# Performance work log

Hardware: AMD Instinct MI355X
Metric: run time of the kernel (lower is better)

Reference implementation:

```python
import jax, jax.numpy as jnp
import numpy as np

B, H, W, C = 16, 64, 64, 192
NUM_HEADS, KEY_DIM, KS = 8, 32, 3


def setup_inputs() -> dict:
    key = jax.random.key(0)
    ks = jax.random.split(key, 9)
    Ck = C + 2  # key/value input dim: patches concat 2 dist channels
    def w(k, shape, fan_in):
        return jax.random.normal(k, shape, jnp.float32) / np.float32(np.sqrt(fan_in))
    return {
        "x": jax.random.normal(ks[0], (B, H, W, C), jnp.float32),
        "Wq": w(ks[1], (C, NUM_HEADS, KEY_DIM), C),
        "bq": jnp.zeros((NUM_HEADS, KEY_DIM), jnp.float32),
        "Wk": w(ks[2], (Ck, NUM_HEADS, KEY_DIM), Ck),
        "bk": jnp.zeros((NUM_HEADS, KEY_DIM), jnp.float32),
        "Wv": w(ks[3], (Ck, NUM_HEADS, KEY_DIM), Ck),
        "bv": jnp.zeros((NUM_HEADS, KEY_DIM), jnp.float32),
        "Wo": w(ks[4], (NUM_HEADS, KEY_DIM, C), NUM_HEADS * KEY_DIM),
        "bo": jnp.zeros((C,), jnp.float32),
    }


def _local_window_kv(x, ks):
    # tf.image.extract_patches SAME (zero pad) -> [B,H,W,ks*ks,C]
    pad = ks // 2
    xp = jnp.pad(x, ((0, 0), (pad, pad), (pad, pad), (0, 0)))
    b, h, w, c = x.shape
    patches = jnp.stack(
        [xp[:, i:i + h, j:j + w, :] for i in range(ks) for j in range(ks)], axis=3
    )  # [B,H,W,ks*ks,C], row-major over window like extract_patches
    # relative distances: tf.meshgrid default 'xy', concat (dists[0], dists[1])
    r = jnp.arange(ks, dtype=x.dtype) - ks // 2
    dx, dy = jnp.meshgrid(r, r)  # 'xy' indexing, matches tf.meshgrid default
    dists = jnp.stack([dx, dy], axis=-1).reshape(ks * ks, 2)  # [9,2]
    dists = jnp.broadcast_to(dists, (b, h, w, ks * ks, 2))
    return jnp.concatenate([patches, dists], axis=-1)  # [B,H,W,9,C+2]


def reference(x, Wq, bq, Wk, bk, Wv, bv, Wo, bo):
    kv_in = _local_window_kv(x, KS)  # [B,H,W,9,C+2]
    # keras MultiHeadAttention projections
    q = jnp.einsum('bxyc,chd->bxyhd', x, Wq) + bq           # [B,H,W,h,d] (q_len=1)
    k = jnp.einsum('bxykc,chd->bxykhd', kv_in, Wk) + bk     # [B,H,W,9,h,d]
    v = jnp.einsum('bxykc,chd->bxykhd', kv_in, Wv) + bv
    scale = np.float32(1.0 / np.sqrt(KEY_DIM))
    scores = jnp.einsum('bxyhd,bxykhd->bxyhk', q, k) * scale  # [B,H,W,h,9]
    attn = jax.nn.softmax(scores, axis=-1)
    o = jnp.einsum('bxyhk,bxykhd->bxyhd', attn, v)
    return jnp.einsum('bxyhd,hdc->bxyc', o, Wo) + bo          # [B,H,W,C]
```

## Files before the change

kernel.cpp:

```cpp
#include <hip/hip_runtime.h>
#include <hip/hip_bf16.h>


typedef __bf16 bf16x8_t __attribute__((ext_vector_type(8)));
typedef float f32x4_t __attribute__((ext_vector_type(4)));

#define SCALE 0.17677669529663687f
#define QSTRIDE 864
#define ZROW 65536

static __device__ __forceinline__ unsigned short bfbits(float f) {
    return __builtin_bit_cast(unsigned short, __float2bfloat16(f));
}
static __device__ __forceinline__ float bf2f(unsigned short u) {
    return __bfloat162float(__builtin_bit_cast(__hip_bfloat16, u));
}
static __device__ __forceinline__ float lo16f(unsigned int u) {
    return __builtin_bit_cast(float, u << 16);
}
static __device__ __forceinline__ float hi16f(unsigned int u) {
    return __builtin_bit_cast(float, u & 0xffff0000u);
}

static __device__ __forceinline__ void gload_lds16(const void* g, void* l) {
    __builtin_amdgcn_global_load_lds((const __attribute__((address_space(1))) void*)g,
                                     (__attribute__((address_space(3))) void*)l, 16, 0, 0);
}

__global__ void k_convert_x(const float* __restrict__ x, ushort4* __restrict__ xb, int n4) {
    int i = blockIdx.x * blockDim.x + threadIdx.x;
    const int stride = gridDim.x * blockDim.x;
    const float4* x4 = reinterpret_cast<const float4*>(x);
    for (; i < n4; i += stride) {
        float4 v = x4[i];
        ushort4 o;
        o.x = bfbits(v.x); o.y = bfbits(v.y); o.z = bfbits(v.z); o.w = bfbits(v.w);
        xb[i] = o;
    }
}

__global__ void k_pack(const float* __restrict__ Wq, const float* __restrict__ Wk,
                       const float* __restrict__ Wv, const float* __restrict__ Wo,
                       const float* __restrict__ bq, const float* __restrict__ bk,
                       const float* __restrict__ bv,
                       __hip_bfloat16* __restrict__ WqkvT, __hip_bfloat16* __restrict__ WoT,
                       float* __restrict__ qkvBias, float* __restrict__ wvTab,
                       __hip_bfloat16* __restrict__ QKV) {
    const int idx = blockIdx.x * blockDim.x + threadIdx.x;
    const int T0 = 896 * 192;
    const int T1 = T0 + 192 * 256;
    const int T2 = T1 + 896;
    const int T3 = T2 + 768;
    const int T4 = T3 + QSTRIDE;
    if (idx < T0) {
        const int m = idx / 192, k = idx % 192;
        float v = 0.f;
        if (m < 256) {
            v = Wq[k * 256 + m] * SCALE;
        } else if (m < 768) {
            const int j = m - 256, g = j >> 3, r = j & 7;
            const int d = 4 * g + (r & 3);
            v = (r < 4) ? Wk[k * 256 + d] : Wv[k * 256 + d];
        } else if (m < 864) {
            const int j = m - 768, h = j / 12, n = j % 12;
            if (n < 9) {
                const float dj = (float)(n % 3 - 1), di = (float)(n / 3 - 1);
                float acc = 0.f;
                for (int d = 0; d < 32; ++d) {
                    const int c = h * 32 + d;
                    const float bkv = dj * Wk[192 * 256 + c] + di * Wk[193 * 256 + c] + bk[c];
                    acc += Wq[k * 256 + c] * bkv;
                }
                v = acc * SCALE;
            }
        }
        WqkvT[m * 192 + k] = __float2bfloat16(v);
    } else if (idx < T1) {
        const int j = idx - T0;
        const int c = j >> 8, hd = j & 255;
        WoT[j] = __float2bfloat16(Wo[hd * 192 + c]);
    } else if (idx < T2) {
        const int col = idx - T1;
        float v = 0.f;
        if (col < 256) v = bq[col] * SCALE;
        else if (col >= 768 && col < 864) {
            const int j = col - 768, h = j / 12, n = j % 12;
            if (n < 9) {
                const float dj = (float)(n % 3 - 1), di = (float)(n / 3 - 1);
                float acc = 0.f;
                for (int d = 0; d < 32; ++d) {
                    const int c = h * 32 + d;
                    const float bkv = dj * Wk[192 * 256 + c] + di * Wk[193 * 256 + c] + bk[c];
                    acc += bq[c] * bkv;
                }
                v = acc * SCALE;
            }
        }
        qkvBias[col] = v;
    } else if (idx < T3) {
        const int j = idx - T2;
        const int t = j >> 8, m = j & 255;
        float v;
        if (t == 0)      v = Wv[192 * 256 + m];
        else if (t == 1) v = Wv[193 * 256 + m];
        else             v = bv[m];
        wvTab[j] = v;
    } else if (idx < T4) {
        const int j = idx - T3;
        QKV[(size_t)ZROW * QSTRIDE + j] = __float2bfloat16(0.f);
    }
}

template<int BM, int BN, int WRN, int WCN, int KDIM, int NOUT, int NBX, bool OUTF32, bool BIAS>
__global__ __launch_bounds__(64 * WRN * WCN) void k_gemm_lds(const __hip_bfloat16* __restrict__ A,
                          const __hip_bfloat16* __restrict__ BT,
                          void* __restrict__ Cout,
                          const float* __restrict__ bias, int ldc) {
    constexpr int NW = WRN * WCN;
    constexpr int WTR = BM / WRN;
    constexpr int WTC = BN / WCN;
    constexpr int FR = WTR / 16;
    constexpr int FC = WTC / 16;
    constexpr int NK = KDIM / 64;
    __shared__ __hip_bfloat16 sA[BM * 64];
    __shared__ __hip_bfloat16 sB[BN * 64];
    const int bid = blockIdx.x;
    const int s = (bid & 7) * ((int)gridDim.x >> 3) + (bid >> 3);
    const int by = s / NBX, bx = s - by * NBX;
    const int tid = threadIdx.x;
    const int wave = tid >> 6, lane = tid & 63;
    const int wr = wave / WCN, wc = wave % WCN;
    const long rowBase = (long)by * BM;
    const long colBase = (long)bx * BN;
    const int lr = lane & 15, lk = lane >> 4;
    const int rx = lr & 7;
    const int srow = lane >> 3;
    const int scolsw = ((lane & 7) ^ srow) * 8;

    f32x4_t acc[FR][FC] = {};
    for (int t = 0; t < NK; ++t) {
        const int k0 = t * 64;
        #pragma unroll
        for (int r = 0; r < BM / (8 * NW); ++r) {
            const int row0 = r * (8 * NW) + wave * 8;
            gload_lds16(A + (rowBase + row0 + srow) * KDIM + k0 + scolsw, sA + row0 * 64);
        }
        #pragma unroll
        for (int r = 0; r < BN / (8 * NW) + ((BN % (8 * NW)) ? 1 : 0); ++r) {
            const int row0 = r * (8 * NW) + wave * 8;
            if (row0 < BN)
                gload_lds16(BT + (colBase + row0 + srow) * KDIM + k0 + scolsw, sB + row0 * 64);
        }
        __syncthreads();
        #pragma unroll
        for (int kk = 0; kk < 2; ++kk) {
            const int pc = ((lk + kk * 4) ^ rx) * 8;
            bf16x8_t a[FR], b[FC];
            #pragma unroll
            for (int fr = 0; fr < FR; ++fr)
                a[fr] = *reinterpret_cast<const bf16x8_t*>(sA + (wr * WTR + fr * 16 + lr) * 64 + pc);
            #pragma unroll
            for (int fc = 0; fc < FC; ++fc)
                b[fc] = *reinterpret_cast<const bf16x8_t*>(sB + (wc * WTC + fc * 16 + lr) * 64 + pc);
            #pragma unroll
            for (int fr = 0; fr < FR; ++fr) {
                #pragma unroll
                for (int fc = 0; fc < FC; ++fc)
                    acc[fr][fc] = __builtin_amdgcn_mfma_f32_16x16x32_bf16(a[fr], b[fc], acc[fr][fc], 0, 0, 0);
            }
        }
        __syncthreads();
    }
    const int rowSub = (lane >> 4) * 4;
    const int colSub = lane & 15;
    #pragma unroll
    for (int fr = 0; fr < FR; ++fr) {
        #pragma unroll
        for (int fc = 0; fc < FC; ++fc) {
            const long col = colBase + wc * WTC + fc * 16 + colSub;
            if (col >= NOUT) continue;
            float bvv = BIAS ? bias[col] : 0.f;
            #pragma unroll
            for (int r = 0; r < 4; ++r) {
                const long row = rowBase + wr * WTR + fr * 16 + rowSub + r;
                float v = acc[fr][fc][r] + bvv;
                if constexpr (OUTF32) ((float*)Cout)[row * ldc + col] = v;
                else ((__hip_bfloat16*)Cout)[row * ldc + col] = __float2bfloat16(v);
            }
        }
    }
}

__global__ __launch_bounds__(256) void k_attn(const __hip_bfloat16* __restrict__ QKV,
                       const float* __restrict__ wvTab,
                       __hip_bfloat16* __restrict__ O) {
    const int wave = threadIdx.x >> 6;
    const int lane = threadIdx.x & 63;
    const int bid = blockIdx.x;
    const int sblk = (bid & 7) * 512 + (bid >> 3);
    const int qd = sblk * 4 + wave;
    const int b = qd >> 10;
    const int qy = (qd >> 5) & 31, qx = qd & 31;
    const int y = qy << 1, x = qx << 1;
    const int p00 = (b << 12) | (y << 6) | x;
    const int h = lane >> 3, dg = lane & 7;
    const int idx = h * 32 + dg * 4;
    const char* baseQ = reinterpret_cast<const char*>(QKV);
    const int laneOff = 512 + 128 * h + 16 * dg;

    uint4 kv[16];
    #pragma unroll
    for (int m = 0; m < 16; ++m) {
        const int rr = m >> 2, cc = m & 3;
        const int ny = y + rr - 1, nx = x + cc - 1;
        const bool inb = ((unsigned)ny < 64u) & ((unsigned)nx < 64u);
        const long row = inb ? (long)((b << 12) | (ny << 6) | nx) : (long)ZROW;
        kv[m] = *reinterpret_cast<const uint4*>(baseQ + row * (QSTRIDE * 2) + laneOff);
    }

    const float4 w0 = *reinterpret_cast<const float4*>(wvTab + idx);
    const float4 w1 = *reinterpret_cast<const float4*>(wvTab + 256 + idx);
    const float4 w2 = *reinterpret_cast<const float4*>(wvTab + 512 + idx);

    #pragma unroll
    for (int pxi = 0; pxi < 4; ++pxi) {
        const int dy = pxi >> 1, dx = pxi & 1;
        const int p = p00 + dy * 64 + dx;
        const __hip_bfloat16* rowQ = QKV + (size_t)p * QSTRIDE;
        const ushort4 qu = *reinterpret_cast<const ushort4*>(rowQ + idx);
        const ushort4 qa = *reinterpret_cast<const ushort4*>(rowQ + 768 + 12 * h);
        const ushort4 qbv = *reinterpret_cast<const ushort4*>(rowQ + 772 + 12 * h);
        const unsigned short qc = *reinterpret_cast<const unsigned short*>(rowQ + 776 + 12 * h);
        const float q0 = bf2f(qu.x), q1 = bf2f(qu.y), q2 = bf2f(qu.z), q3 = bf2f(qu.w);
        const float qb[9] = { bf2f(qa.x), bf2f(qa.y), bf2f(qa.z), bf2f(qa.w),
                              bf2f(qbv.x), bf2f(qbv.y), bf2f(qbv.z), bf2f(qbv.w), bf2f(qc) };

        float sc[9];
        #pragma unroll
        for (int n = 0; n < 9; ++n) {
            const int m = (dy + n / 3) * 4 + dx + n % 3;
            const uint4 k = kv[m];
            float s = fmaf(q0, lo16f(k.x), fmaf(q1, hi16f(k.x),
                      fmaf(q2, lo16f(k.y), q3 * hi16f(k.y))));
            s += __shfl_xor(s, 1);
            s += __shfl_xor(s, 2);
            s += __shfl_xor(s, 4);
            sc[n] = s + qb[n];
        }
        float mx = sc[0];
        #pragma unroll
        for (int n = 1; n < 9; ++n) mx = fmaxf(mx, sc[n]);
        float sum = 0.f;
        #pragma unroll
        for (int n = 0; n < 9; ++n) { sc[n] = __expf(sc[n] - mx); sum += sc[n]; }
        const float inv = 1.0f / sum;
        const float Ej = (sc[2] + sc[5] + sc[8]) - (sc[0] + sc[3] + sc[6]);
        const float Ei = (sc[6] + sc[7] + sc[8]) - (sc[0] + sc[1] + sc[2]);

        float o0 = 0.f, o1 = 0.f, o2 = 0.f, o3 = 0.f;
        #pragma unroll
        for (int n = 0; n < 9; ++n) {
            const int m = (dy + n / 3) * 4 + dx + n % 3;
            const uint4 k = kv[m];
            o0 = fmaf(sc[n], lo16f(k.z), o0);
            o1 = fmaf(sc[n], hi16f(k.z), o1);
            o2 = fmaf(sc[n], lo16f(k.w), o2);
            o3 = fmaf(sc[n], hi16f(k.w), o3);
        }
        ushort4 ov;
        ov.x = bfbits(fmaf(Ej, w0.x, fmaf(Ei, w1.x, o0)) * inv + w2.x);
        ov.y = bfbits(fmaf(Ej, w0.y, fmaf(Ei, w1.y, o1)) * inv + w2.y);
        ov.z = bfbits(fmaf(Ej, w0.z, fmaf(Ei, w1.z, o2)) * inv + w2.z);
        ov.w = bfbits(fmaf(Ej, w0.w, fmaf(Ei, w1.w, o3)) * inv + w2.w);
        *reinterpret_cast<ushort4*>(O + (size_t)p * 256 + idx) = ov;
    }
}

extern "C" void kernel_launch(void* const* d_in, const int* in_sizes, int n_in,
                              void* d_out, int out_size, void* d_ws, size_t ws_size,
                              hipStream_t stream) {
    (void)in_sizes; (void)n_in; (void)out_size; (void)ws_size;
    const float* x  = (const float*)d_in[0];
    const float* Wq = (const float*)d_in[1];
    const float* bq = (const float*)d_in[2];
    const float* Wk = (const float*)d_in[3];
    const float* bk = (const float*)d_in[4];
    const float* Wv = (const float*)d_in[5];
    const float* bv = (const float*)d_in[6];
    const float* Wo = (const float*)d_in[7];
    const float* bo = (const float*)d_in[8];

    char* ws = (char*)d_ws;
    __hip_bfloat16* xb    = (__hip_bfloat16*)(ws + 0);
    __hip_bfloat16* O     = (__hip_bfloat16*)(ws + 0);
    __hip_bfloat16* QKV   = (__hip_bfloat16*)(ws + 33554432);
    __hip_bfloat16* WqkvT = (__hip_bfloat16*)(ws + 146802368);
    __hip_bfloat16* WoT   = (__hip_bfloat16*)(ws + 147146432);
    float* qkvBias        = (float*)(ws + 147244736);
    float* wvTab          = (float*)(ws + 147248320);

    k_convert_x<<<4096, 256, 0, stream>>>(x, (ushort4*)xb, 12582912 / 4);
    k_pack<<<874, 256, 0, stream>>>(Wq, Wk, Wv, Wo, bq, bk, bv, WqkvT, WoT, qkvBias, wvTab, QKV);
    k_gemm_lds<128, 128, 2, 4, 192, 864, 7, false, true>
        <<<3584, 512, 0, stream>>>(xb, WqkvT, (void*)QKV, qkvBias, QSTRIDE);
    k_attn<<<4096, 256, 0, stream>>>(QKV, wvTab, O);
    k_gemm_lds<128, 64, 2, 4, 256, 192, 3, true, true>
        <<<1536, 512, 0, stream>>>(O, WoT, d_out, bo, 192);
}
```

Measured before the change: 110.7 us.

## Fuse output projection into attention kernel via LDS-staged MFMA

```diff
diff --git a/kernel.cpp b/kernel.cpp
--- a/kernel.cpp
+++ b/kernel.cpp
@@ -191,9 +191,12 @@
     }
 }
 
-__global__ __launch_bounds__(256) void k_attn(const __hip_bfloat16* __restrict__ QKV,
+__global__ __launch_bounds__(256) void k_attn_out(const __hip_bfloat16* __restrict__ QKV,
                        const float* __restrict__ wvTab,
-                       __hip_bfloat16* __restrict__ O) {
+                       const __hip_bfloat16* __restrict__ WoT,
+                       const float* __restrict__ bo,
+                       float* __restrict__ out) {
+    __shared__ __hip_bfloat16 oS[16][264];
     const int wave = threadIdx.x >> 6;
     const int lane = threadIdx.x & 63;
     const int bid = blockIdx.x;
@@ -272,7 +275,37 @@
         ov.y = bfbits(fmaf(Ej, w0.y, fmaf(Ei, w1.y, o1)) * inv + w2.y);
         ov.z = bfbits(fmaf(Ej, w0.z, fmaf(Ei, w1.z, o2)) * inv + w2.z);
         ov.w = bfbits(fmaf(Ej, w0.w, fmaf(Ei, w1.w, o3)) * inv + w2.w);
-        *reinterpret_cast<ushort4*>(O + (size_t)p * 256 + idx) = ov;
+        *reinterpret_cast<ushort4*>(&oS[wave * 4 + pxi][idx]) = ov;
+    }
+    __syncthreads();
+
+    const int lr = lane & 15, lk = lane >> 4;
+    f32x4_t acc[3] = {};
+    #pragma unroll
+    for (int k = 0; k < 8; ++k) {
+        const bf16x8_t a = *reinterpret_cast<const bf16x8_t*>(&oS[lr][k * 32 + lk * 8]);
+        #pragma unroll
+        for (int t = 0; t < 3; ++t) {
+            const int col = (wave * 3 + t) * 16 + lr;
+            const bf16x8_t bfr = *reinterpret_cast<const bf16x8_t*>(WoT + col * 256 + k * 32 + lk * 8);
+            acc[t] = __builtin_amdgcn_mfma_f32_16x16x32_bf16(a, bfr, acc[t], 0, 0, 0);
+        }
+    }
+    const int g = lane >> 4;
+    const int qd2 = sblk * 4 + g;
+    const int b2 = qd2 >> 10;
+    const int y2 = ((qd2 >> 5) & 31) << 1;
+    const int x2 = (qd2 & 31) << 1;
+    const int pbase = (b2 << 12) | (y2 << 6) | x2;
+    #pragma unroll
+    for (int t = 0; t < 3; ++t) {
+        const int col = (wave * 3 + t) * 16 + (lane & 15);
+        const float bov = bo[col];
+        #pragma unroll
+        for (int r = 0; r < 4; ++r) {
+            const int p = pbase + (r >> 1) * 64 + (r & 1);
+            out[(size_t)p * 192 + col] = acc[t][r] + bov;
+        }
     }
 }
 
@@ -292,7 +325,6 @@
 
     char* ws = (char*)d_ws;
     __hip_bfloat16* xb    = (__hip_bfloat16*)(ws + 0);
-    __hip_bfloat16* O     = (__hip_bfloat16*)(ws + 0);
     __hip_bfloat16* QKV   = (__hip_bfloat16*)(ws + 33554432);
     __hip_bfloat16* WqkvT = (__hip_bfloat16*)(ws + 146802368);
     __hip_bfloat16* WoT   = (__hip_bfloat16*)(ws + 147146432);
@@ -303,7 +335,5 @@
     k_pack<<<874, 256, 0, stream>>>(Wq, Wk, Wv, Wo, bq, bk, bv, WqkvT, WoT, qkvBias, wvTab, QKV);
     k_gemm_lds<128, 128, 2, 4, 192, 864, 7, false, true>
         <<<3584, 512, 0, stream>>>(xb, WqkvT, (void*)QKV, qkvBias, QSTRIDE);
-    k_attn<<<4096, 256, 0, stream>>>(QKV, wvTab, O);
-    k_gemm_lds<128, 64, 2, 4, 256, 192, 3, true, true>
-        <<<1536, 512, 0, stream>>>(O, WoT, d_out, bo, 192);
-}
+    k_attn_out<<<4096, 256, 0, stream>>>(QKV, wvTab, WoT, bo, (float*)d_out);
+}
```

After: 131.5 us. 1.19x slower.
